# Kernel optimization log

Hardware: AMD Instinct MI355X
Metric: run time of the kernel (lower is better)

Reference implementation:

```python
import jax, jax.numpy as jnp
import numpy as np

B, S, H, NH = 4, 2048, 1024, 16
HD = H // NH

def setup_inputs() -> dict:
    key = jax.random.key(0)
    ks = jax.random.split(key, 11)
    std = 1.0 / np.sqrt(H)
    inp = {
        'query': jax.random.normal(ks[0], (B, S, H), dtype=jnp.float32),
        'key':   jax.random.normal(ks[1], (B, S, H), dtype=jnp.float32),
        'value': jax.random.normal(ks[2], (B, S, H), dtype=jnp.float32),
        'Wq': jax.random.uniform(ks[3], (H, H), jnp.float32, -std, std),
        'bq': jax.random.uniform(ks[4], (H,), jnp.float32, -std, std),
        'Wk': jax.random.uniform(ks[5], (H, H), jnp.float32, -std, std),
        'bk': jax.random.uniform(ks[6], (H,), jnp.float32, -std, std),
        'Wv': jax.random.uniform(ks[7], (H, H), jnp.float32, -std, std),
        'bv': jax.random.uniform(ks[8], (H,), jnp.float32, -std, std),
        'Wo': jax.random.uniform(ks[9], (H, H), jnp.float32, -std, std),
        'bo': jax.random.uniform(ks[10], (H,), jnp.float32, -std, std),
    }
    return inp

def reference(query, key, value, Wq, bq, Wk, bk, Wv, bv, Wo, bo):
    def split_heads(x):  # [B,S,H] -> [B,NH,S,HD]
        return x.reshape(B, -1, NH, HD).transpose(0, 2, 1, 3)
    Q = split_heads(query @ Wq.T + bq)
    K = split_heads(key @ Wk.T + bk)
    V = split_heads(value @ Wv.T + bv)
    scores = jnp.einsum('bhqd,bhkd->bhqk', Q, K) / np.sqrt(HD).astype(np.float32)
    weights = jax.nn.softmax(scores, axis=-1)
    attn = jnp.einsum('bhqk,bhkd->bhqd', weights, V)  # [B,NH,S,HD]
    attn = attn.transpose(0, 2, 1, 3).reshape(B, -1, H)
    return attn @ Wo.T + bo
```

## Files before the change

kernel.cpp:

```cpp
#include <hip/hip_runtime.h>
#include <hip/hip_bf16.h>

typedef __attribute__((ext_vector_type(4)))  float f32x4;
typedef __attribute__((ext_vector_type(16))) float f32x16;
typedef __attribute__((ext_vector_type(8)))  short bf16x8;
typedef __attribute__((ext_vector_type(4)))  short bf16x4;

#define DEVI static __device__ __forceinline__

constexpr int Bn = 4, Sn = 2048, Hn = 1024, NHn = 16, HDn = 64;
constexpr int Kn = 1024, Nn = 1024;
constexpr float QSCALE = 0.18033688011112042f;

DEVI unsigned short f2bf(float x) {
    union { float f; unsigned u; } v; v.f = x;
    unsigned r = v.u + 0x7fffu + ((v.u >> 16) & 1u);
    return (unsigned short)(r >> 16);
}

DEVI f32x4 mfma16(bf16x8 a, bf16x8 b, f32x4 c) {
    return __builtin_amdgcn_mfma_f32_16x16x32_bf16(a, b, c, 0, 0, 0);
}
DEVI f32x16 mfma32(bf16x8 a, bf16x8 b, f32x16 c) {
    return __builtin_amdgcn_mfma_f32_32x32x16_bf16(a, b, c, 0, 0, 0);
}
DEVI unsigned cvt_pk_bf16(float lo, float hi) {
    unsigned r;
    asm("v_cvt_pk_bf16_f32 %0, %1, %2" : "=v"(r) : "v"(lo), "v"(hi));
    return r;
}
DEVI void pl32swap(unsigned &a, unsigned &b) {
    asm("v_permlane32_swap_b32 %0, %1" : "+v"(a), "+v"(b));
}
DEVI float exp2_raw(float x) { return __builtin_amdgcn_exp2f(x); }

typedef const __attribute__((address_space(1))) void* gas1_t;
typedef __attribute__((address_space(3))) void* gas3_t;

__global__ void convert_w_kernel(const float* __restrict__ w0, const float* __restrict__ w1,
                                 const float* __restrict__ w2, const float* __restrict__ w3,
                                 unsigned short* __restrict__ out)
{
    int mat = blockIdx.x >> 10;
    int i4  = ((blockIdx.x & 1023) << 8) + threadIdx.x;
    const float* w = mat == 0 ? w0 : mat == 1 ? w1 : mat == 2 ? w2 : w3;
    f32x4 v = *reinterpret_cast<const f32x4*>(w + (size_t)i4 * 4);
    union { unsigned u[2]; bf16x4 s; } pk;
    pk.u[0] = cvt_pk_bf16(v[0], v[1]);
    pk.u[1] = cvt_pk_bf16(v[2], v[3]);
    *reinterpret_cast<bf16x4*>(out + (((size_t)mat) << 20) + (size_t)i4 * 4) = pk.s;
}

template<bool A_BF16>
DEVI void gemm_body(const void* __restrict__ Av, const unsigned short* __restrict__ Bw,
                    const float* __restrict__ bias, void* __restrict__ Out,
                    float scale, int out_mode)
{
    __shared__ __align__(16) unsigned short As[128 * 32];
    __shared__ __align__(16) unsigned short Bs[128 * 32];

    const int tid = threadIdx.x;
    const int wid = tid >> 6, lane = tid & 63;
    const int lhi = lane >> 4, llo = lane & 15;
    const int bid = blockIdx.x;
    const int sid = (bid & 7) * 64 + (bid >> 3);
    const int bx = sid & 7;
    const int by = sid >> 3;
    const int brow = by * 128, bcol = bx * 128;
    const int wr = wid >> 1, wc = wid & 1;

    f32x4 acc[4][4] = {};

    for (int kt = 0; kt < Kn / 32; ++kt) {
        __syncthreads();
        #pragma unroll
        for (int r = 0; r < 2; ++r) {
            int lin = r * 256 + tid;
            int row = lin >> 2, kc = (lin & 3) * 8;
            const unsigned short* g = Bw + (size_t)(bcol + row) * Kn + kt * 32 + kc;
            unsigned short* ldst = Bs + (size_t)(r * 256 + wid * 64) * 8;
            __builtin_amdgcn_global_load_lds((gas1_t)g, (gas3_t)ldst, 16, 0, 0);
        }
        if constexpr (A_BF16) {
            const unsigned short* A = (const unsigned short*)Av;
            #pragma unroll
            for (int r = 0; r < 2; ++r) {
                int lin = r * 256 + tid;
                int row = lin >> 2, kc = (lin & 3) * 8;
                const unsigned short* g = A + (size_t)(brow + row) * Kn + kt * 32 + kc;
                unsigned short* ldst = As + (size_t)(r * 256 + wid * 64) * 8;
                __builtin_amdgcn_global_load_lds((gas1_t)g, (gas3_t)ldst, 16, 0, 0);
            }
        } else {
            const float* A = (const float*)Av;
            #pragma unroll
            for (int r = 0; r < 4; ++r) {
                int lin = r * 256 + tid;
                int row = lin >> 3, kc = (lin & 7) * 4;
                f32x4 v = *reinterpret_cast<const f32x4*>(A + (size_t)(brow + row) * Kn + kt * 32 + kc);
                union { unsigned u[2]; bf16x4 s; } pk;
                pk.u[0] = cvt_pk_bf16(v[0], v[1]);
                pk.u[1] = cvt_pk_bf16(v[2], v[3]);
                *reinterpret_cast<bf16x4*>(As + row * 32 + kc) = pk.s;
            }
        }
        __syncthreads();

        bf16x8 a[4], b[4];
        #pragma unroll
        for (int m = 0; m < 4; ++m)
            a[m] = *reinterpret_cast<const bf16x8*>(As + (wr * 64 + m * 16 + llo) * 32 + lhi * 8);
        #pragma unroll
        for (int n = 0; n < 4; ++n)
            b[n] = *reinterpret_cast<const bf16x8*>(Bs + (wc * 64 + n * 16 + llo) * 32 + lhi * 8);
        #pragma unroll
        for (int m = 0; m < 4; ++m)
            #pragma unroll
            for (int n = 0; n < 4; ++n)
                acc[m][n] = mfma16(a[m], b[n], acc[m][n]);
    }

    #pragma unroll
    for (int m = 0; m < 4; ++m) {
        #pragma unroll
        for (int n = 0; n < 4; ++n) {
            const int col  = bcol + wc * 64 + n * 16 + llo;
            const int row0 = brow + wr * 64 + m * 16 + lhi * 4;
            const float bv = bias[col];
            if (out_mode == 0) {
                unsigned short* O = (unsigned short*)Out;
                const int h = col >> 6, d = col & 63;
                #pragma unroll
                for (int r = 0; r < 4; ++r) {
                    int rowm = row0 + r;
                    int bb = rowm >> 11, ss = rowm & 2047;
                    O[((((size_t)bb * NHn + h) * Sn + ss) << 6) + d] =
                        f2bf((acc[m][n][r] + bv) * scale);
                }
            } else if (out_mode == 1) {
                unsigned short* O = (unsigned short*)Out;
                const int h = col >> 6, d = col & 63;
                const int bb = row0 >> 11, ss = row0 & 2047;
                union { unsigned u[2]; bf16x4 s; } pk;
                pk.u[0] = cvt_pk_bf16(acc[m][n][0] + bv, acc[m][n][1] + bv);
                pk.u[1] = cvt_pk_bf16(acc[m][n][2] + bv, acc[m][n][3] + bv);
                *reinterpret_cast<bf16x4*>(O + (((size_t)bb * NHn + h) * HDn + d) * Sn + ss) = pk.s;
            } else {
                float* O = (float*)Out;
                #pragma unroll
                for (int r = 0; r < 4; ++r)
                    O[(size_t)(row0 + r) * Nn + col] = acc[m][n][r] + bv;
            }
        }
    }
}

__global__ __launch_bounds__(256, 2)
void qkv_proj_kernel(const float* __restrict__ xq, const float* __restrict__ xk,
                     const float* __restrict__ xv, const unsigned short* __restrict__ Wb,
                     const float* __restrict__ bq, const float* __restrict__ bk,
                     const float* __restrict__ bv,
                     unsigned short* __restrict__ Qw, unsigned short* __restrict__ Kw,
                     unsigned short* __restrict__ Vw)
{
    const int z = blockIdx.z;
    const float* A           = z == 0 ? xq : z == 1 ? xk : xv;
    const unsigned short* W  = Wb + (((size_t)z) << 20);
    const float* bias        = z == 0 ? bq : z == 1 ? bk : bv;
    unsigned short* Out      = z == 0 ? Qw : z == 1 ? Kw : Vw;
    const float scale        = z == 0 ? QSCALE : 1.0f;
    const int mode           = z == 2 ? 1 : 0;
    gemm_body<false>(A, W, bias, Out, scale, mode);
}

__global__ __launch_bounds__(256, 2)
void out_proj_kernel(const unsigned short* __restrict__ attn, const unsigned short* __restrict__ Wo,
                     const float* __restrict__ bo, float* __restrict__ out)
{
    gemm_body<true>(attn, Wo, bo, out, 1.0f, 2);
}

__global__ __launch_bounds__(256, 2)
void attn_kernel(const unsigned short* __restrict__ Q, const unsigned short* __restrict__ K,
                 const unsigned short* __restrict__ Vt, unsigned short* __restrict__ On)
{
    __shared__ __align__(16) unsigned short LDST[2 * 2 * 4096];

    const int tid = threadIdx.x;
    const int wid = tid >> 6, lane = tid & 63;
    const int l31 = lane & 31, h = lane >> 5;
    const int bid = blockIdx.x;
    const int sid = (bid & 7) * 64 + (bid >> 3);
    const int bh = sid >> 3;
    const int qt = sid & 7;
    const int q0 = qt * 256 + wid * 64;

    const unsigned short* Qb = Q + (size_t)bh * Sn * HDn;
    const unsigned short* Kb = K + (size_t)bh * Sn * HDn;
    const unsigned short* Vb = Vt + (size_t)bh * HDn * Sn;

    int koff[2], voff[2];
    #pragma unroll
    for (int r = 0; r < 2; ++r) {
        int lin = (r * 256 + tid) * 16;
        int row = lin >> 7, colb = lin & 127;
        int scolb = colb ^ ((row & 7) << 4);
        koff[r] = row * HDn + (scolb >> 1);
        voff[r] = row * Sn + (scolb >> 1);
    }

    auto stage = [&](int buf, int key0) {
        #pragma unroll
        for (int r = 0; r < 2; ++r)
            __builtin_amdgcn_global_load_lds((gas1_t)(Kb + koff[r] + key0 * HDn),
                (gas3_t)(LDST + buf * 8192 + r * 2048 + wid * 512), 16, 0, 0);
        #pragma unroll
        for (int r = 0; r < 2; ++r)
            __builtin_amdgcn_global_load_lds((gas1_t)(Vb + voff[r] + key0),
                (gas3_t)(LDST + buf * 8192 + 4096 + r * 2048 + wid * 512), 16, 0, 0);
    };

    auto rdT = [&](int byteoff) -> bf16x8 {
        return *reinterpret_cast<const bf16x8*>((const char*)LDST + byteoff);
    };
    const int lrow = l31 * 128;
    const int lswz = (l31 & 7) << 4;

    bf16x8 qfA[4], qfB[4];
    #pragma unroll
    for (int sd = 0; sd < 4; ++sd) {
        qfA[sd] = *reinterpret_cast<const bf16x8*>(Qb + (size_t)(q0 + l31) * HDn + sd * 16 + h * 8);
        qfB[sd] = *reinterpret_cast<const bf16x8*>(Qb + (size_t)(q0 + 32 + l31) * HDn + sd * 16 + h * 8);
    }

    bf16x8 ones;
    #pragma unroll
    for (int i = 0; i < 8; ++i) ones[i] = (short)0x3F80;

    f32x16 oA0 = {}, oA1 = {}, oB0 = {}, oB1 = {};
    f32x16 lsA = {}, lsB = {};

    stage(0, 0);
    __syncthreads();

    auto body = [&](int buf) {
        const int base = buf * 16384;
        bf16x8 ka0[4], ka1[4];
        #pragma unroll
        for (int sd = 0; sd < 4; ++sd) {
            int la = lrow + ((sd * 32 + h * 16) ^ lswz);
            ka0[sd] = rdT(base + la);
            ka1[sd] = rdT(base + 4096 + la);
        }
        f32x16 sA0 = {}, sA1 = {}, sB0 = {}, sB1 = {};
        __builtin_amdgcn_s_setprio(1);
        #pragma unroll
        for (int sd = 0; sd < 4; ++sd) sA0 = mfma32(ka0[sd], qfA[sd], sA0);
        #pragma unroll
        for (int sd = 0; sd < 4; ++sd) sA1 = mfma32(ka1[sd], qfA[sd], sA1);
        #pragma unroll
        for (int sd = 0; sd < 4; ++sd) sB0 = mfma32(ka0[sd], qfB[sd], sB0);
        #pragma unroll
        for (int sd = 0; sd < 4; ++sd) sB1 = mfma32(ka1[sd], qfB[sd], sB1);
        __builtin_amdgcn_s_setprio(0);

        bf16x8 va0[4], va1[4];
        #pragma unroll
        for (int S = 0; S < 4; ++S) {
            int la = lrow + ((S * 32 + h * 16) ^ lswz);
            va0[S] = rdT(base + 8192 + la);
            va1[S] = rdT(base + 8192 + 4096 + la);
        }

        #pragma unroll
        for (int r = 0; r < 16; ++r) {
            sA0[r] = exp2_raw(sA0[r]); sA1[r] = exp2_raw(sA1[r]);
            sB0[r] = exp2_raw(sB0[r]); sB1[r] = exp2_raw(sB1[r]);
        }

        unsigned WpA[2][4][2], WpB[2][4][2];
        #pragma unroll
        for (int R = 0; R < 4; ++R) {
            WpA[0][R][0] = cvt_pk_bf16(sA0[4 * R],     sA0[4 * R + 1]);
            WpA[0][R][1] = cvt_pk_bf16(sA0[4 * R + 2], sA0[4 * R + 3]);
            WpA[1][R][0] = cvt_pk_bf16(sA1[4 * R],     sA1[4 * R + 1]);
            WpA[1][R][1] = cvt_pk_bf16(sA1[4 * R + 2], sA1[4 * R + 3]);
            WpB[0][R][0] = cvt_pk_bf16(sB0[4 * R],     sB0[4 * R + 1]);
            WpB[0][R][1] = cvt_pk_bf16(sB0[4 * R + 2], sB0[4 * R + 3]);
            WpB[1][R][0] = cvt_pk_bf16(sB1[4 * R],     sB1[4 * R + 1]);
            WpB[1][R][1] = cvt_pk_bf16(sB1[4 * R + 2], sB1[4 * R + 3]);
        }

        #pragma unroll
        for (int kc = 0; kc < 2; ++kc) {
            #pragma unroll
            for (int sp = 0; sp < 2; ++sp) {
                const int S = kc * 2 + sp;
                unsigned a0 = WpA[kc][2 * sp][0], a2 = WpA[kc][2 * sp + 1][0];
                unsigned a1 = WpA[kc][2 * sp][1], a3 = WpA[kc][2 * sp + 1][1];
                pl32swap(a0, a2);
                pl32swap(a1, a3);
                union { unsigned u[4]; bf16x8 v; } pbA;
                pbA.u[0] = a0; pbA.u[1] = a1; pbA.u[2] = a2; pbA.u[3] = a3;
                unsigned b0 = WpB[kc][2 * sp][0], b2 = WpB[kc][2 * sp + 1][0];
                unsigned b1 = WpB[kc][2 * sp][1], b3 = WpB[kc][2 * sp + 1][1];
                pl32swap(b0, b2);
                pl32swap(b1, b3);
                union { unsigned u[4]; bf16x8 v; } pbB;
                pbB.u[0] = b0; pbB.u[1] = b1; pbB.u[2] = b2; pbB.u[3] = b3;
                __builtin_amdgcn_s_setprio(1);
                oA0 = mfma32(va0[S], pbA.v, oA0);
                oA1 = mfma32(va1[S], pbA.v, oA1);
                lsA = mfma32(ones,   pbA.v, lsA);
                oB0 = mfma32(va0[S], pbB.v, oB0);
                oB1 = mfma32(va1[S], pbB.v, oB1);
                lsB = mfma32(ones,   pbB.v, lsB);
                __builtin_amdgcn_s_setprio(0);
            }
        }
    };

    constexpr int NT = Sn / 64;
    for (int kt = 0; kt < NT; kt += 2) {
        stage(1, (kt + 1) * 64);
        body(0);
        __syncthreads();
        if (kt + 2 < NT) stage(0, (kt + 2) * 64);
        body(1);
        __syncthreads();
    }

    const float invA = 1.f / lsA[0], invB = 1.f / lsB[0];
    const int b = bh >> 4, hh = bh & 15;
    unsigned short* OrowA = On + ((size_t)b * Sn + (q0 + l31))      * Hn + hh * 64;
    unsigned short* OrowB = On + ((size_t)b * Sn + (q0 + 32 + l31)) * Hn + hh * 64;
    #pragma unroll
    for (int g = 0; g < 4; ++g) {
        union { unsigned u[2]; bf16x4 s; } pA0, pA1, pB0, pB1;
        pA0.u[0] = cvt_pk_bf16(oA0[4 * g] * invA,     oA0[4 * g + 1] * invA);
        pA0.u[1] = cvt_pk_bf16(oA0[4 * g + 2] * invA, oA0[4 * g + 3] * invA);
        pA1.u[0] = cvt_pk_bf16(oA1[4 * g] * invA,     oA1[4 * g + 1] * invA);
        pA1.u[1] = cvt_pk_bf16(oA1[4 * g + 2] * invA, oA1[4 * g + 3] * invA);
        pB0.u[0] = cvt_pk_bf16(oB0[4 * g] * invB,     oB0[4 * g + 1] * invB);
        pB0.u[1] = cvt_pk_bf16(oB0[4 * g + 2] * invB, oB0[4 * g + 3] * invB);
        pB1.u[0] = cvt_pk_bf16(oB1[4 * g] * invB,     oB1[4 * g + 1] * invB);
        pB1.u[1] = cvt_pk_bf16(oB1[4 * g + 2] * invB, oB1[4 * g + 3] * invB);
        *reinterpret_cast<bf16x4*>(OrowA + g * 8 + 4 * h)      = pA0.s;
        *reinterpret_cast<bf16x4*>(OrowA + 32 + g * 8 + 4 * h) = pA1.s;
        *reinterpret_cast<bf16x4*>(OrowB + g * 8 + 4 * h)      = pB0.s;
        *reinterpret_cast<bf16x4*>(OrowB + 32 + g * 8 + 4 * h) = pB1.s;
    }
}

extern "C" void kernel_launch(void* const* d_in, const int* in_sizes, int n_in,
                              void* d_out, int out_size, void* d_ws, size_t ws_size,
                              hipStream_t stream)
{
    (void)in_sizes; (void)n_in; (void)out_size;
    const float* q  = (const float*)d_in[0];
    const float* k  = (const float*)d_in[1];
    const float* v  = (const float*)d_in[2];
    const float* Wq = (const float*)d_in[3];
    const float* bq = (const float*)d_in[4];
    const float* Wk = (const float*)d_in[5];
    const float* bk = (const float*)d_in[6];
    const float* Wv = (const float*)d_in[7];
    const float* bv = (const float*)d_in[8];
    const float* Wo = (const float*)d_in[9];
    const float* bo = (const float*)d_in[10];
    float* out = (float*)d_out;

    if (ws_size < (size_t)72 * 1024 * 1024) return;

    unsigned short* Wb = (unsigned short*)d_ws;
    unsigned short* Qw = Wb + (size_t)4 * 1024 * 1024;
    unsigned short* Kw = Qw + (size_t)8 * 1024 * 1024;
    unsigned short* Vw = Kw + (size_t)8 * 1024 * 1024;
    unsigned short* Aw = Vw + (size_t)8 * 1024 * 1024;

    convert_w_kernel<<<4096, 256, 0, stream>>>(Wq, Wk, Wv, Wo, Wb);
    qkv_proj_kernel<<<dim3(512, 1, 3), 256, 0, stream>>>(q, k, v, Wb, bq, bk, bv, Qw, Kw, Vw);
    attn_kernel<<<512, 256, 0, stream>>>(Qw, Kw, Vw, Aw);
    out_proj_kernel<<<512, 256, 0, stream>>>(Aw, Wb + ((size_t)3 << 20), bo, out);
}
```

Baseline: 198.3 us.

## Double-buffer QKV projection and compute softmax row sums with VALU

The QKV projection kernel now double-buffers its LDS tiles. It issues the fp32 A loads and the B global-to-LDS loads for the next k-tile before the MFMAs on the current one, so global latency overlaps compute. The attention kernel stops computing row sums with an extra MFMA against a ones vector and instead adds the exponentiated scores in registers, then combines the two half-waves with a shuffle. This cuts matrix-core work by a third in the PV loop, but adds VALU adds, doubles LDS in the projection kernel, and raises register pressure.

```diff
diff --git a/kernel.cpp b/kernel.cpp
--- a/kernel.cpp
+++ b/kernel.cpp
@@ -51,10 +51,9 @@
     *reinterpret_cast<bf16x4*>(out + (((size_t)mat) << 20) + (size_t)i4 * 4) = pk.s;
 }
 
-template<bool A_BF16>
-DEVI void gemm_body(const void* __restrict__ Av, const unsigned short* __restrict__ Bw,
-                    const float* __restrict__ bias, void* __restrict__ Out,
-                    float scale, int out_mode)
+__global__ __launch_bounds__(256, 2)
+void out_proj_kernel(const unsigned short* __restrict__ Aw, const unsigned short* __restrict__ Bw,
+                     const float* __restrict__ bias, float* __restrict__ Out)
 {
     __shared__ __align__(16) unsigned short As[128 * 32];
     __shared__ __align__(16) unsigned short Bs[128 * 32];
@@ -64,8 +63,7 @@
     const int lhi = lane >> 4, llo = lane & 15;
     const int bid = blockIdx.x;
     const int sid = (bid & 7) * 64 + (bid >> 3);
-    const int bx = sid & 7;
-    const int by = sid >> 3;
+    const int bx = sid & 7, by = sid >> 3;
     const int brow = by * 128, bcol = bx * 128;
     const int wr = wid >> 1, wc = wid & 1;
 
@@ -77,32 +75,17 @@
         for (int r = 0; r < 2; ++r) {
             int lin = r * 256 + tid;
             int row = lin >> 2, kc = (lin & 3) * 8;
-            const unsigned short* g = Bw + (size_t)(bcol + row) * Kn + kt * 32 + kc;
-            unsigned short* ldst = Bs + (size_t)(r * 256 + wid * 64) * 8;
-            __builtin_amdgcn_global_load_lds((gas1_t)g, (gas3_t)ldst, 16, 0, 0);
-        }
-        if constexpr (A_BF16) {
-            const unsigned short* A = (const unsigned short*)Av;
-            #pragma unroll
-            for (int r = 0; r < 2; ++r) {
-                int lin = r * 256 + tid;
-                int row = lin >> 2, kc = (lin & 3) * 8;
-                const unsigned short* g = A + (size_t)(brow + row) * Kn + kt * 32 + kc;
-                unsigned short* ldst = As + (size_t)(r * 256 + wid * 64) * 8;
-                __builtin_amdgcn_global_load_lds((gas1_t)g, (gas3_t)ldst, 16, 0, 0);
-            }
-        } else {
-            const float* A = (const float*)Av;
-            #pragma unroll
-            for (int r = 0; r < 4; ++r) {
-                int lin = r * 256 + tid;
-                int row = lin >> 3, kc = (lin & 7) * 4;
-                f32x4 v = *reinterpret_cast<const f32x4*>(A + (size_t)(brow + row) * Kn + kt * 32 + kc);
-                union { unsigned u[2]; bf16x4 s; } pk;
-                pk.u[0] = cvt_pk_bf16(v[0], v[1]);
-                pk.u[1] = cvt_pk_bf16(v[2], v[3]);
-                *reinterpret_cast<bf16x4*>(As + row * 32 + kc) = pk.s;
-            }
+            __builtin_amdgcn_global_load_lds(
+                (gas1_t)(Bw + (size_t)(bcol + row) * Kn + kt * 32 + kc),
+                (gas3_t)(Bs + (size_t)(r * 256 + wid * 64) * 8), 16, 0, 0);
+        }
+        #pragma unroll
+        for (int r = 0; r < 2; ++r) {
+            int lin = r * 256 + tid;
+            int row = lin >> 2, kc = (lin & 3) * 8;
+            __builtin_amdgcn_global_load_lds(
+                (gas1_t)(Aw + (size_t)(brow + row) * Kn + kt * 32 + kc),
+                (gas3_t)(As + (size_t)(r * 256 + wid * 64) * 8), 16, 0, 0);
         }
         __syncthreads();
 
@@ -121,38 +104,16 @@
     }
 
     #pragma unroll
-    for (int m = 0; m < 4; ++m) {
+    for (int m = 0; m < 4; ++m)
         #pragma unroll
         for (int n = 0; n < 4; ++n) {
             const int col  = bcol + wc * 64 + n * 16 + llo;
             const int row0 = brow + wr * 64 + m * 16 + lhi * 4;
             const float bv = bias[col];
-            if (out_mode == 0) {
-                unsigned short* O = (unsigned short*)Out;
-                const int h = col >> 6, d = col & 63;
-                #pragma unroll
-                for (int r = 0; r < 4; ++r) {
-                    int rowm = row0 + r;
-                    int bb = rowm >> 11, ss = rowm & 2047;
-                    O[((((size_t)bb * NHn + h) * Sn + ss) << 6) + d] =
-                        f2bf((acc[m][n][r] + bv) * scale);
-                }
-            } else if (out_mode == 1) {
-                unsigned short* O = (unsigned short*)Out;
-                const int h = col >> 6, d = col & 63;
-                const int bb = row0 >> 11, ss = row0 & 2047;
-                union { unsigned u[2]; bf16x4 s; } pk;
-                pk.u[0] = cvt_pk_bf16(acc[m][n][0] + bv, acc[m][n][1] + bv);
-                pk.u[1] = cvt_pk_bf16(acc[m][n][2] + bv, acc[m][n][3] + bv);
-                *reinterpret_cast<bf16x4*>(O + (((size_t)bb * NHn + h) * HDn + d) * Sn + ss) = pk.s;
-            } else {
-                float* O = (float*)Out;
-                #pragma unroll
-                for (int r = 0; r < 4; ++r)
-                    O[(size_t)(row0 + r) * Nn + col] = acc[m][n][r] + bv;
-            }
-        }
-    }
+            #pragma unroll
+            for (int r = 0; r < 4; ++r)
+                Out[(size_t)(row0 + r) * Nn + col] = acc[m][n][r] + bv;
+        }
 }
 
 __global__ __launch_bounds__(256, 2)
@@ -163,21 +124,118 @@
                      unsigned short* __restrict__ Qw, unsigned short* __restrict__ Kw,
                      unsigned short* __restrict__ Vw)
 {
+    __shared__ __align__(16) unsigned short As[2][128 * 32];
+    __shared__ __align__(16) unsigned short Bs[2][128 * 32];
+
     const int z = blockIdx.z;
     const float* A           = z == 0 ? xq : z == 1 ? xk : xv;
     const unsigned short* W  = Wb + (((size_t)z) << 20);
     const float* bias        = z == 0 ? bq : z == 1 ? bk : bv;
     unsigned short* Out      = z == 0 ? Qw : z == 1 ? Kw : Vw;
     const float scale        = z == 0 ? QSCALE : 1.0f;
-    const int mode           = z == 2 ? 1 : 0;
-    gemm_body<false>(A, W, bias, Out, scale, mode);
-}
-
-__global__ __launch_bounds__(256, 2)
-void out_proj_kernel(const unsigned short* __restrict__ attn, const unsigned short* __restrict__ Wo,
-                     const float* __restrict__ bo, float* __restrict__ out)
-{
-    gemm_body<true>(attn, Wo, bo, out, 1.0f, 2);
+
+    const int tid = threadIdx.x;
+    const int wid = tid >> 6, lane = tid & 63;
+    const int lhi = lane >> 4, llo = lane & 15;
+    const int bid = blockIdx.x;
+    const int sid = (bid & 7) * 64 + (bid >> 3);
+    const int bx = sid & 7, by = sid >> 3;
+    const int brow = by * 128, bcol = bx * 128;
+    const int wr = wid >> 1, wc = wid & 1;
+
+    f32x4 acc[4][4] = {};
+
+    auto issueA = [&](f32x4 (&ar)[4], int kt) {
+        #pragma unroll
+        for (int r = 0; r < 4; ++r) {
+            int lin = r * 256 + tid;
+            int row = lin >> 3, kc = (lin & 7) * 4;
+            ar[r] = *reinterpret_cast<const f32x4*>(A + (size_t)(brow + row) * Kn + kt * 32 + kc);
+        }
+    };
+    auto stageB = [&](int buf, int kt) {
+        #pragma unroll
+        for (int r = 0; r < 2; ++r) {
+            int lin = r * 256 + tid;
+            int row = lin >> 2, kc = (lin & 3) * 8;
+            __builtin_amdgcn_global_load_lds(
+                (gas1_t)(W + (size_t)(bcol + row) * Kn + kt * 32 + kc),
+                (gas3_t)(Bs[buf] + (size_t)(r * 256 + wid * 64) * 8), 16, 0, 0);
+        }
+    };
+    auto writeA = [&](int buf, f32x4 (&ar)[4]) {
+        #pragma unroll
+        for (int r = 0; r < 4; ++r) {
+            int lin = r * 256 + tid;
+            int row = lin >> 3, kc = (lin & 7) * 4;
+            union { unsigned u[2]; bf16x4 s; } pk;
+            pk.u[0] = cvt_pk_bf16(ar[r][0], ar[r][1]);
+            pk.u[1] = cvt_pk_bf16(ar[r][2], ar[r][3]);
+            *reinterpret_cast<bf16x4*>(As[buf] + row * 32 + kc) = pk.s;
+        }
+    };
+    auto compute = [&](int buf) {
+        bf16x8 a[4], b[4];
+        #pragma unroll
+        for (int m = 0; m < 4; ++m)
+            a[m] = *reinterpret_cast<const bf16x8*>(As[buf] + (wr * 64 + m * 16 + llo) * 32 + lhi * 8);
+        #pragma unroll
+        for (int n = 0; n < 4; ++n)
+            b[n] = *reinterpret_cast<const bf16x8*>(Bs[buf] + (wc * 64 + n * 16 + llo) * 32 + lhi * 8);
+        #pragma unroll
+        for (int m = 0; m < 4; ++m)
+            #pragma unroll
+            for (int n = 0; n < 4; ++n)
+                acc[m][n] = mfma16(a[m], b[n], acc[m][n]);
+    };
+
+    constexpr int NKT = Kn / 32;
+    f32x4 ar0[4], ar1[4];
+
+    issueA(ar0, 0);
+    stageB(0, 0);
+    writeA(0, ar0);
+    __syncthreads();
+
+    for (int kt = 0; kt < NKT; kt += 2) {
+        issueA(ar1, kt + 1);
+        stageB(1, kt + 1);
+        compute(0);
+        writeA(1, ar1);
+        __syncthreads();
+        if (kt + 2 < NKT) { issueA(ar0, kt + 2); stageB(0, kt + 2); }
+        compute(1);
+        if (kt + 2 < NKT) writeA(0, ar0);
+        __syncthreads();
+    }
+
+    #pragma unroll
+    for (int m = 0; m < 4; ++m) {
+        #pragma unroll
+        for (int n = 0; n < 4; ++n) {
+            const int col  = bcol + wc * 64 + n * 16 + llo;
+            const int row0 = brow + wr * 64 + m * 16 + lhi * 4;
+            const float bv = bias[col];
+            const int hh = col >> 6, d = col & 63;
+            if (z != 2) {
+                unsigned short* O = (unsigned short*)Out;
+                #pragma unroll
+                for (int r = 0; r < 4; ++r) {
+                    int rowm = row0 + r;
+                    int bb = rowm >> 11, ss = rowm & 2047;
+                    O[((((size_t)bb * NHn + hh) * Sn + ss) << 6) + d] =
+                        f2bf((acc[m][n][r] + bv) * scale);
+                }
+            } else {
+                unsigned short* O = (unsigned short*)Out;
+                const int bb = row0 >> 11, ss = row0 & 2047;
+                union { unsigned u[2]; bf16x4 s; } pk;
+                pk.u[0] = cvt_pk_bf16(acc[m][n][0] + bv, acc[m][n][1] + bv);
+                pk.u[1] = cvt_pk_bf16(acc[m][n][2] + bv, acc[m][n][3] + bv);
+                *reinterpret_cast<bf16x4*>(O + (((size_t)bb * NHn + hh) * HDn + d) * Sn + ss) = pk.s;
+            }
+        }
+    }
 }
 
 __global__ __launch_bounds__(256, 2)
@@ -233,12 +291,8 @@
         qfB[sd] = *reinterpret_cast<const bf16x8*>(Qb + (size_t)(q0 + 32 + l31) * HDn + sd * 16 + h * 8);
     }
 
-    bf16x8 ones;
-    #pragma unroll
-    for (int i = 0; i < 8; ++i) ones[i] = (short)0x3F80;
-
     f32x16 oA0 = {}, oA1 = {}, oB0 = {}, oB1 = {};
-    f32x16 lsA = {}, lsB = {};
+    float lA = 0.f, lB = 0.f;
 
     stage(0, 0);
     __syncthreads();
@@ -276,6 +330,19 @@
         for (int r = 0; r < 16; ++r) {
             sA0[r] = exp2_raw(sA0[r]); sA1[r] = exp2_raw(sA1[r]);
             sB0[r] = exp2_raw(sB0[r]); sB1[r] = exp2_raw(sB1[r]);
+        }
+
+        {
+            float sa[16], sb[16];
+            #pragma unroll
+            for (int r = 0; r < 16; ++r) { sa[r] = sA0[r] + sA1[r]; sb[r] = sB0[r] + sB1[r]; }
+            #pragma unroll
+            for (int st = 8; st > 0; st >>= 1)
+                #pragma unroll
+                for (int r = 0; r < 8; ++r)
+                    if (r < st) { sa[r] += sa[r + st]; sb[r] += sb[r + st]; }
+            lA += sa[0];
+            lB += sb[0];
         }
 
         unsigned WpA[2][4][2], WpB[2][4][2];
@@ -311,10 +378,8 @@
                 __builtin_amdgcn_s_setprio(1);
                 oA0 = mfma32(va0[S], pbA.v, oA0);
                 oA1 = mfma32(va1[S], pbA.v, oA1);
-                lsA = mfma32(ones,   pbA.v, lsA);
                 oB0 = mfma32(va0[S], pbB.v, oB0);
                 oB1 = mfma32(va1[S], pbB.v, oB1);
-                lsB = mfma32(ones,   pbB.v, lsB);
                 __builtin_amdgcn_s_setprio(0);
             }
         }
@@ -330,7 +395,9 @@
         __syncthreads();
     }
 
-    const float invA = 1.f / lsA[0], invB = 1.f / lsB[0];
+    lA += __shfl_xor(lA, 32, 64);
+    lB += __shfl_xor(lB, 32, 64);
+    const float invA = 1.f / lA, invB = 1.f / lB;
     const int b = bh >> 4, hh = bh & 15;
     unsigned short* OrowA = On + ((size_t)b * Sn + (q0 + l31))      * Hn + hh * 64;
     unsigned short* OrowB = On + ((size_t)b * Sn + (q0 + 32 + l31)) * Hn + hh * 64;
```

After: 185.5 us (median of 2 runs). 6.4% less time.
